# Optimization experiments

Measured on AMD Instinct MI355X. Metric: run time of the kernel, lower is better.

The kernel has to match this reference:

```python
import jax, jax.numpy as jnp
import numpy as np

N, D_IN = 65536, 512
X_DIMS = [512, 2048, 2048, 512]
Y_DIMS = [512, 1024, 512]
T = 2            # n_treatments
OUT_DIM = 1


def setup_inputs() -> dict:
    key = jax.random.key(0)
    ks = iter(jax.random.split(key, 32))
    s = 0.02
    inp = {
        "x": jax.random.normal(next(ks), (N, D_IN), dtype=jnp.float32),
        "treatment": jax.random.randint(next(ks), (N,), 0, T, dtype=jnp.int64),
        # shared trunk MLP (Linear+ReLU after EVERY linear, per original code)
        "Wx0": jax.random.normal(next(ks), (X_DIMS[0], X_DIMS[1]), jnp.float32) * s,
        "bx0": jnp.zeros((X_DIMS[1],), jnp.float32),
        "Wx1": jax.random.normal(next(ks), (X_DIMS[1], X_DIMS[2]), jnp.float32) * s,
        "bx1": jnp.zeros((X_DIMS[2],), jnp.float32),
        "Wx2": jax.random.normal(next(ks), (X_DIMS[2], X_DIMS[3]), jnp.float32) * s,
        "bx2": jnp.zeros((X_DIMS[3],), jnp.float32),
        # per-treatment expert MLPs, stacked on leading T axis
        "Wy0": jax.random.normal(next(ks), (T, Y_DIMS[0], Y_DIMS[1]), jnp.float32) * s,
        "by0": jnp.zeros((T, Y_DIMS[1]), jnp.float32),
        "Wy1": jax.random.normal(next(ks), (T, Y_DIMS[1], Y_DIMS[2]), jnp.float32) * s,
        "by1": jnp.zeros((T, Y_DIMS[2]), jnp.float32),
        # per-treatment output heads
        "Wo": jax.random.normal(next(ks), (T, Y_DIMS[2], OUT_DIM), jnp.float32) * s,
        "bo": jnp.zeros((T, OUT_DIM), jnp.float32),
        # propensity head
        "Wt": jax.random.normal(next(ks), (X_DIMS[3], 1), jnp.float32) * s,
        "bt": jnp.zeros((1,), jnp.float32),
    }
    return inp


def reference(x, treatment, Wx0, bx0, Wx1, bx1, Wx2, bx2,
              Wy0, by0, Wy1, by1, Wo, bo, Wt, bt):
    # shared trunk: ReLU follows every Linear (original MLP applies ReLU after
    # the last layer too, because `i < len(dims)-1` is always true in the loop)
    h = jax.nn.relu(x @ Wx0 + bx0)
    h = jax.nn.relu(h @ Wx1 + bx1)
    x_emb = jax.nn.relu(h @ Wx2 + bx2)            # [N, 512]

    # per-treatment experts computed densely, then gathered by treatment id.
    # This is the dense-equivalent of SplitStreams -> MLP -> GatherStreams:
    # GatherStreams sorts by original row index, so row n of the output is the
    # treatment-`t[n]` head applied to x_emb[n].
    g = jax.nn.relu(jnp.einsum('nd,tdh->nth', x_emb, Wy0) + by0)   # [N,T,1024]
    g = jax.nn.relu(jnp.einsum('nth,thk->ntk', g, Wy1) + by1)      # [N,T,512]
    y_all = jnp.einsum('ntk,tko->nto', g, Wo) + bo                 # [N,T,1]

    t_idx = treatment.astype(jnp.int32).reshape(-1)
    y = jnp.take_along_axis(y_all, t_idx[:, None, None], axis=1)[:, 0, :]  # [N,1]

    # softmax over a size-1 axis -> all ones, but kept faithful to the source
    t_out = jax.nn.softmax(x_emb @ Wt + bt, axis=1)                # [N,1]
    return y, x_emb, t_out
```

## Files before the change

### kernel.cpp

```cpp
#include <hip/hip_runtime.h>
#include <hip/hip_bf16.h>
#include <cstdint>

#define NROWS 65536
#define TTREAT 2

typedef __bf16 bf16x8 __attribute__((ext_vector_type(8)));
typedef float f32x4 __attribute__((ext_vector_type(4)));
typedef unsigned short u16;
typedef u16 u16x8 __attribute__((ext_vector_type(8)));

#define GLOBAL_AS __attribute__((address_space(1)))
#define LDS_AS __attribute__((address_space(3)))

__device__ __forceinline__ u16 f32_to_bf16_bits(float f) {
    union { float f; uint32_t u; } v; v.f = f;
    uint32_t u = v.u;
    return (u16)((u + 0x7FFFu + ((u >> 16) & 1u)) >> 16);
}

__device__ __forceinline__ float bf16_bits_to_f32(u16 b) {
    union { uint32_t u; float f; } v; v.u = ((uint32_t)b) << 16;
    return v.f;
}

__global__ void cvt_f32_bf16(const float4* __restrict__ src, u16x8* __restrict__ dst, int n8) {
    int i = blockIdx.x * blockDim.x + threadIdx.x;
    if (i >= n8) return;
    float4 a = src[2 * i], b = src[2 * i + 1];
    u16x8 r;
    r[0] = f32_to_bf16_bits(a.x); r[1] = f32_to_bf16_bits(a.y);
    r[2] = f32_to_bf16_bits(a.z); r[3] = f32_to_bf16_bits(a.w);
    r[4] = f32_to_bf16_bits(b.x); r[5] = f32_to_bf16_bits(b.y);
    r[6] = f32_to_bf16_bits(b.z); r[7] = f32_to_bf16_bits(b.w);
    dst[i] = r;
}

__global__ void transpose_w(const float* __restrict__ src, u16* __restrict__ dst, int K, int M) {
    __shared__ float tile[32][33];
    size_t boff = (size_t)blockIdx.z * K * M;
    src += boff; dst += boff;
    int m0 = blockIdx.x * 32, k0 = blockIdx.y * 32;
    int tx = threadIdx.x, ty = threadIdx.y;
#pragma unroll
    for (int i = 0; i < 32; i += 8)
        tile[ty + i][tx] = src[(size_t)(k0 + ty + i) * M + m0 + tx];
    __syncthreads();
#pragma unroll
    for (int i = 0; i < 32; i += 8)
        dst[(size_t)(m0 + ty + i) * K + k0 + tx] = f32_to_bf16_bits(tile[tx][ty + i]);
}

__global__ void zero_cnt(int* cnt) {
    if (threadIdx.x < TTREAT) cnt[threadIdx.x] = 0;
}

__global__ void partition_rows(const int* __restrict__ treat, int* __restrict__ idx, int* __restrict__ cnt) {
    __shared__ int waveCnt1[4];
    __shared__ int blockBase[2];
    const int tid = threadIdx.x;
    const int i = blockIdx.x * 256 + tid;
    const int wave = tid >> 6, lane = tid & 63;
    const int t = treat[i];
    const unsigned long long m1 = __ballot(t == 1);
    const int n1 = __popcll(m1);
    if (lane == 0) waveCnt1[wave] = n1;
    __syncthreads();
    const int w0 = waveCnt1[0], w1 = waveCnt1[1], w2 = waveCnt1[2], w3 = waveCnt1[3];
    const int tot1 = w0 + w1 + w2 + w3;
    if (tid == 0) blockBase[0] = atomicAdd(&cnt[0], 256 - tot1);
    else if (tid == 64) blockBase[1] = atomicAdd(&cnt[1], tot1);
    __syncthreads();
    int waveOff1 = 0;
    if (wave > 0) waveOff1 += w0;
    if (wave > 1) waveOff1 += w1;
    if (wave > 2) waveOff1 += w2;
    const int below1 = (int)__popcll(m1 & ((1ull << lane) - 1ull));
    int pos;
    if (t == 1) pos = blockBase[1] + waveOff1 + below1;
    else        pos = blockBase[0] + (wave * 64 - waveOff1) + (lane - below1);
    idx[t * NROWS + pos] = i;
}

template <bool GATHER, bool WRITE_F32>
__global__ void gemm_bias_relu(const u16* __restrict__ A, const u16* __restrict__ Bt,
                               const float* __restrict__ bias,
                               u16* __restrict__ C, float* __restrict__ C32,
                               const int* __restrict__ idx, const int* __restrict__ cntp,
                               int nrows, int chunkStart, int maxRows, int K, int M) {
    int rows = (cntp ? *cntp : nrows) - chunkStart;
    if (rows > maxRows) rows = maxRows;
    int rowBase = blockIdx.y * 128;
    if (rows <= 0 || rowBase >= rows) return;
    int colBase = blockIdx.x * 128;

    __shared__ __align__(16) u16 As[128 * 64];
    __shared__ __align__(16) u16 Bs[128 * 64];

    const int tid = threadIdx.x;
    const int wave = tid >> 6, lane = tid & 63;
    const int quad = lane >> 4, l16 = lane & 15;
    const int wm = wave >> 1, wn = wave & 1;

    const int r0 = tid >> 3;
    const int kc = (tid & 7) * 8;

    size_t a_off[4], b_off[4];
#pragma unroll
    for (int it = 0; it < 4; ++it) {
        int r = rowBase + r0 + it * 32;
        int grow;
        if (GATHER) {
            int rc = r < rows ? r : (rows - 1);
            grow = idx[rc];
        } else {
            grow = r;
        }
        a_off[it] = (size_t)grow * K + kc;
        int c = colBase + r0 + it * 32;
        b_off[it] = (size_t)c * K + kc;
    }

    f32x4 acc[4][4] = {};

    for (int k0 = 0; k0 < K; k0 += 64) {
        __syncthreads();
#pragma unroll
        for (int it = 0; it < 4; ++it) {
            __builtin_amdgcn_global_load_lds(
                (const GLOBAL_AS void*)(A + a_off[it] + k0),
                (LDS_AS void*)(&As[(it * 256 + wave * 64) * 8]), 16, 0, 0);
            __builtin_amdgcn_global_load_lds(
                (const GLOBAL_AS void*)(Bt + b_off[it] + k0),
                (LDS_AS void*)(&Bs[(it * 256 + wave * 64) * 8]), 16, 0, 0);
        }
        __syncthreads();
#pragma unroll
        for (int kk = 0; kk < 2; ++kk) {
            bf16x8 aF[4], bF[4];
            const int ko = kk * 32 + quad * 8;
#pragma unroll
            for (int mi = 0; mi < 4; ++mi)
                aF[mi] = *(const bf16x8*)&As[(wm * 64 + mi * 16 + l16) * 64 + ko];
#pragma unroll
            for (int ni = 0; ni < 4; ++ni)
                bF[ni] = *(const bf16x8*)&Bs[(wn * 64 + ni * 16 + l16) * 64 + ko];
#pragma unroll
            for (int mi = 0; mi < 4; ++mi)
#pragma unroll
                for (int ni = 0; ni < 4; ++ni)
                    acc[mi][ni] = __builtin_amdgcn_mfma_f32_16x16x32_bf16(
                        aF[mi], bF[ni], acc[mi][ni], 0, 0, 0);
        }
    }

    float bv[4];
#pragma unroll
    for (int ni = 0; ni < 4; ++ni) bv[ni] = bias[colBase + wn * 64 + ni * 16 + l16];

#pragma unroll
    for (int mi = 0; mi < 4; ++mi) {
        int rloc = rowBase + wm * 64 + mi * 16 + quad * 4;
#pragma unroll
        for (int ni = 0; ni < 4; ++ni) {
            int col = colBase + wn * 64 + ni * 16 + l16;
#pragma unroll
            for (int r = 0; r < 4; ++r) {
                int row = rloc + r;
                if (row < rows) {
                    float v = acc[mi][ni][r] + bv[ni];
                    v = v > 0.f ? v : 0.f;
                    C[(size_t)row * M + col] = f32_to_bf16_bits(v);
                    if (WRITE_F32) C32[(size_t)row * M + col] = v;
                }
            }
        }
    }
}

__global__ void head_kernel(const u16* __restrict__ g2, const int* __restrict__ idx,
                            const int* __restrict__ cntp, int chunkStart, int maxRows,
                            const float* __restrict__ Wo,
                            const float* __restrict__ bo, float* __restrict__ y) {
    int rows = *cntp - chunkStart;
    if (rows > maxRows) rows = maxRows;
    int wave = threadIdx.x >> 6, lane = threadIdx.x & 63;
    int pos = blockIdx.x * 4 + wave;
    if (pos >= rows) return;
    const u16* grow = g2 + (size_t)pos * 512;
    u16x8 gv = *(const u16x8*)&grow[lane * 8];
    const float4* w4 = (const float4*)Wo + lane * 2;
    float4 w0 = w4[0], w1 = w4[1];
    float s = 0.f;
    s += bf16_bits_to_f32(gv[0]) * w0.x + bf16_bits_to_f32(gv[1]) * w0.y;
    s += bf16_bits_to_f32(gv[2]) * w0.z + bf16_bits_to_f32(gv[3]) * w0.w;
    s += bf16_bits_to_f32(gv[4]) * w1.x + bf16_bits_to_f32(gv[5]) * w1.y;
    s += bf16_bits_to_f32(gv[6]) * w1.z + bf16_bits_to_f32(gv[7]) * w1.w;
#pragma unroll
    for (int off = 32; off > 0; off >>= 1) s += __shfl_down(s, off);
    if (lane == 0) y[idx[pos]] = s + bo[0];
}

__global__ void ones_kernel(float* __restrict__ dst, int n) {
    int i = blockIdx.x * 256 + threadIdx.x;
    if (i < n) dst[i] = 1.0f;
}

extern "C" void kernel_launch(void* const* d_in, const int* in_sizes, int n_in,
                              void* d_out, int out_size, void* d_ws, size_t ws_size,
                              hipStream_t stream) {
    const float* x   = (const float*)d_in[0];
    const int* treat = (const int*)d_in[1];
    const float* Wx0 = (const float*)d_in[2];
    const float* bx0 = (const float*)d_in[3];
    const float* Wx1 = (const float*)d_in[4];
    const float* bx1 = (const float*)d_in[5];
    const float* Wx2 = (const float*)d_in[6];
    const float* bx2 = (const float*)d_in[7];
    const float* Wy0 = (const float*)d_in[8];
    const float* by0 = (const float*)d_in[9];
    const float* Wy1 = (const float*)d_in[10];
    const float* by1 = (const float*)d_in[11];
    const float* Wo  = (const float*)d_in[12];
    const float* bo  = (const float*)d_in[13];

    float* out_y  = (float*)d_out;
    float* out_xe = out_y + NROWS;
    float* out_t  = out_xe + (size_t)NROWS * 512;

    const size_t FIXED = ((size_t)(2048 * 512 + 2048 * 2048 + 512 * 2048
                          + TTREAT * 1024 * 512 + TTREAT * 512 * 1024
                          + (size_t)NROWS * 512) * 2)
                          + (size_t)TTREAT * NROWS * 4 + (1 << 20);
    int R = 512;
    const int cands[6] = {16384, 8192, 4096, 2048, 1024, 512};
    for (int ci = 0; ci < 6; ++ci) {
        if (FIXED + (size_t)cands[ci] * 12288 <= ws_size) { R = cands[ci]; break; }
    }
    const int NCHUNK = NROWS / R;

    size_t off = 0;
    auto carve = [&](size_t bytes) {
        void* p = (char*)d_ws + off;
        off += (bytes + 255) & ~(size_t)255;
        return p;
    };
    u16* Wx0t = (u16*)carve((size_t)2048 * 512 * 2);
    u16* Wx1t = (u16*)carve((size_t)2048 * 2048 * 2);
    u16* Wx2t = (u16*)carve((size_t)512 * 2048 * 2);
    u16* Wy0t = (u16*)carve((size_t)TTREAT * 1024 * 512 * 2);
    u16* Wy1t = (u16*)carve((size_t)TTREAT * 512 * 1024 * 2);
    u16* xe   = (u16*)carve((size_t)NROWS * 512 * 2);
    int* idx  = (int*)carve((size_t)TTREAT * NROWS * 4);
    int* cnt  = (int*)carve(256);
    u16* xbc  = (u16*)carve((size_t)R * 512 * 2);
    u16* h1c  = (u16*)carve((size_t)R * 2048 * 2);
    u16* h2c  = (u16*)carve((size_t)R * 2048 * 2);
    u16* g1c  = (u16*)carve((size_t)R * 1024 * 2);
    u16* g2c  = (u16*)carve((size_t)R * 512 * 2);

    dim3 tb32(32, 8);

    transpose_w<<<dim3(2048 / 32, 512 / 32, 1), tb32, 0, stream>>>(Wx0, Wx0t, 512, 2048);
    transpose_w<<<dim3(2048 / 32, 2048 / 32, 1), tb32, 0, stream>>>(Wx1, Wx1t, 2048, 2048);
    transpose_w<<<dim3(512 / 32, 2048 / 32, 1), tb32, 0, stream>>>(Wx2, Wx2t, 2048, 512);
    transpose_w<<<dim3(1024 / 32, 512 / 32, TTREAT), tb32, 0, stream>>>(Wy0, Wy0t, 512, 1024);
    transpose_w<<<dim3(512 / 32, 1024 / 32, TTREAT), tb32, 0, stream>>>(Wy1, Wy1t, 1024, 512);

    zero_cnt<<<1, 64, 0, stream>>>(cnt);
    partition_rows<<<NROWS / 256, 256, 0, stream>>>(treat, idx, cnt);

    const int gy = R / 128;

    for (int c = 0; c < NCHUNK; ++c) {
        int cS = c * R;
        cvt_f32_bf16<<<(R * 512 / 8 + 255) / 256, 256, 0, stream>>>(
            (const float4*)(x + (size_t)cS * 512), (u16x8*)xbc, R * 512 / 8);
        gemm_bias_relu<false, false><<<dim3(2048 / 128, gy), 256, 0, stream>>>(
            xbc, Wx0t, bx0, h1c, nullptr, nullptr, nullptr, NROWS, cS, R, 512, 2048);
        gemm_bias_relu<false, false><<<dim3(2048 / 128, gy), 256, 0, stream>>>(
            h1c, Wx1t, bx1, h2c, nullptr, nullptr, nullptr, NROWS, cS, R, 2048, 2048);
        gemm_bias_relu<false, true><<<dim3(512 / 128, gy), 256, 0, stream>>>(
            h2c, Wx2t, bx2, xe + (size_t)cS * 512, out_xe + (size_t)cS * 512,
            nullptr, nullptr, NROWS, cS, R, 2048, 512);
    }

    for (int t = 0; t < TTREAT; ++t) {
        const int* idx_t = idx + (size_t)t * NROWS;
        for (int c = 0; c < NCHUNK; ++c) {
            int cS = c * R;
            gemm_bias_relu<true, false><<<dim3(1024 / 128, gy), 256, 0, stream>>>(
                xe, Wy0t + (size_t)t * 1024 * 512, by0 + (size_t)t * 1024,
                g1c, nullptr, idx_t + cS, cnt + t, NROWS, cS, R, 512, 1024);
            gemm_bias_relu<false, false><<<dim3(512 / 128, gy), 256, 0, stream>>>(
                g1c, Wy1t + (size_t)t * 512 * 1024, by1 + (size_t)t * 512,
                g2c, nullptr, nullptr, cnt + t, NROWS, cS, R, 1024, 512);
            head_kernel<<<R / 4, 256, 0, stream>>>(
                g2c, idx_t + cS, cnt + t, cS, R, Wo + (size_t)t * 512, bo + t, out_y);
        }
    }

    ones_kernel<<<NROWS / 256, 256, 0, stream>>>(out_t, NROWS);
}
```

Baseline: 1.652 ms.

## XOR-swizzle bf16 activations and weights in global memory to avoid LDS bank conflicts

Stores all bf16 operands (converted input, transposed weights, intermediate activations) with an XOR swizzle of 8-element chunks within each 64-column group, keyed by row. The GEMM's direct global-to-LDS loads then land pre-swizzled, and the MFMA fragment reads from LDS use the matching XOR, spreading row accesses across banks. Gathered rows get a combined swizzle, and the head kernel un-swizzles its weight index. This adds index arithmetic and a global-layout dependency across every producer and consumer kernel.

```diff
diff --git a/kernel.cpp b/kernel.cpp
--- a/kernel.cpp
+++ b/kernel.cpp
@@ -12,6 +12,10 @@
 
 #define GLOBAL_AS __attribute__((address_space(1)))
 #define LDS_AS __attribute__((address_space(3)))
+
+__device__ __forceinline__ int swz_col(int col, int row) {
+    return (col & ~63) | (((((col >> 3) & 7) ^ (row & 7)) << 3)) | (col & 7);
+}
 
 __device__ __forceinline__ u16 f32_to_bf16_bits(float f) {
     union { float f; uint32_t u; } v; v.f = f;
@@ -33,7 +37,9 @@
     r[2] = f32_to_bf16_bits(a.z); r[3] = f32_to_bf16_bits(a.w);
     r[4] = f32_to_bf16_bits(b.x); r[5] = f32_to_bf16_bits(b.y);
     r[6] = f32_to_bf16_bits(b.z); r[7] = f32_to_bf16_bits(b.w);
-    dst[i] = r;
+    int row = i >> 6;
+    int j = (i & ~7) | ((i ^ row) & 7);
+    dst[j] = r;
 }
 
 __global__ void transpose_w(const float* __restrict__ src, u16* __restrict__ dst, int K, int M) {
@@ -47,8 +53,10 @@
         tile[ty + i][tx] = src[(size_t)(k0 + ty + i) * M + m0 + tx];
     __syncthreads();
 #pragma unroll
-    for (int i = 0; i < 32; i += 8)
-        dst[(size_t)(m0 + ty + i) * K + k0 + tx] = f32_to_bf16_bits(tile[tx][ty + i]);
+    for (int i = 0; i < 32; i += 8) {
+        int row = m0 + ty + i, col = k0 + tx;
+        dst[(size_t)row * K + swz_col(col, row)] = f32_to_bf16_bits(tile[tx][ty + i]);
+    }
 }
 
 __global__ void zero_cnt(int* cnt) {
@@ -109,14 +117,14 @@
 #pragma unroll
     for (int it = 0; it < 4; ++it) {
         int r = rowBase + r0 + it * 32;
-        int grow;
         if (GATHER) {
             int rc = r < rows ? r : (rows - 1);
-            grow = idx[rc];
+            int g = idx[rc];
+            int kcg = ((((tid & 7) ^ (r & 7) ^ (g & 7)) & 7) * 8);
+            a_off[it] = (size_t)g * K + kcg;
         } else {
-            grow = r;
-        }
-        a_off[it] = (size_t)grow * K + kc;
+            a_off[it] = (size_t)r * K + kc;
+        }
         int c = colBase + r0 + it * 32;
         b_off[it] = (size_t)c * K + kc;
     }
@@ -138,13 +146,13 @@
 #pragma unroll
         for (int kk = 0; kk < 2; ++kk) {
             bf16x8 aF[4], bF[4];
-            const int ko = kk * 32 + quad * 8;
+            const int csw = ((kk * 4 + quad) ^ (l16 & 7)) * 8;
 #pragma unroll
             for (int mi = 0; mi < 4; ++mi)
-                aF[mi] = *(const bf16x8*)&As[(wm * 64 + mi * 16 + l16) * 64 + ko];
+                aF[mi] = *(const bf16x8*)&As[(wm * 64 + mi * 16 + l16) * 64 + csw];
 #pragma unroll
             for (int ni = 0; ni < 4; ++ni)
-                bF[ni] = *(const bf16x8*)&Bs[(wn * 64 + ni * 16 + l16) * 64 + ko];
+                bF[ni] = *(const bf16x8*)&Bs[(wn * 64 + ni * 16 + l16) * 64 + csw];
 #pragma unroll
             for (int mi = 0; mi < 4; ++mi)
 #pragma unroll
@@ -170,7 +178,7 @@
                 if (row < rows) {
                     float v = acc[mi][ni][r] + bv[ni];
                     v = v > 0.f ? v : 0.f;
-                    C[(size_t)row * M + col] = f32_to_bf16_bits(v);
+                    C[(size_t)row * M + swz_col(col, row)] = f32_to_bf16_bits(v);
                     if (WRITE_F32) C32[(size_t)row * M + col] = v;
                 }
             }
@@ -189,7 +197,8 @@
     if (pos >= rows) return;
     const u16* grow = g2 + (size_t)pos * 512;
     u16x8 gv = *(const u16x8*)&grow[lane * 8];
-    const float4* w4 = (const float4*)Wo + lane * 2;
+    int logical = (lane & ~7) | ((lane ^ pos) & 7);
+    const float4* w4 = (const float4*)Wo + logical * 2;
     float4 w0 = w4[0], w1 = w4[1];
     float s = 0.f;
     s += bf16_bits_to_f32(gv[0]) * w0.x + bf16_bits_to_f32(gv[1]) * w0.y;
```

After: 1.548 ms. 1.07x faster.
